# Optimization experiments

Measured on AMD Instinct MI355X. Metric: run time of the kernel, lower is better.

## Reference

```python
import jax, jax.numpy as jnp
import numpy as np
from jax import lax

L = 15      # time_conv_size
STRIDE = 2


def setup_inputs() -> dict:
    key = jax.random.key(0)
    k1, k2, k3 = jax.random.split(key, 3)
    x = jax.random.normal(k1, (8, 4096, 64), dtype=jnp.float32)
    w1 = jax.random.normal(k2, (L,), dtype=jnp.float32)
    w2 = jax.random.normal(k3, (L,), dtype=jnp.float32)
    return {"x": x, "w1": w1, "w2": w2}


def reference(x, w1, w2):
    # x: [B, T, C]; w1, w2: [L]
    B, T, C = x.shape
    p = L // 2
    # --- weighted local mean: mu[b,t,c] = sum_k w1[k] * x_pad[b,t+k,c] ---
    x_pad = jnp.pad(x, ((0, 0), (p, p), (0, 0)))
    mu = sum(w1[k] * x_pad[:, k:k + T, :] for k in range(L))  # [B,T,C]
    # --- centered diagonal bilinear (covariance) pooling ---
    xc_pad = jnp.pad(x - mu, ((0, 0), (p, p), (0, 0)))  # [B, T+2p, C]
    # strided window indices: I = ceil(T/STRIDE) windows of length L
    starts = jnp.arange(0, T, STRIDE)                   # [I]
    idx = starts[:, None] + jnp.arange(L)[None, :]      # [I, L]
    win = xc_pad[:, idx, :]                             # [B, I, L, C]
    sigma = jnp.einsum('bilc,l,bild->bicd', win, w2, win)
    I = starts.shape[0]
    sigma = sigma.reshape(B, I, C * C)
    mu_s = mu[:, ::STRIDE, :]                           # [B, I, C]
    out = jnp.concatenate([mu_s, sigma], axis=-1)       # [B, I, C + C*C]
    # K.l2_normalize over last axis (epsilon=1e-12)
    denom = lax.rsqrt(jnp.maximum(jnp.sum(out * out, axis=-1, keepdims=True), 1e-12))
    return out * denom
```

## Files before the change

kernel.cpp:

```cpp
#include <hip/hip_runtime.h>

#define Tdim 4096
#define Bdim 8
#define Cdim 64
#define Ldim 15
#define Idim 2048
#define OUTW 4160
#define G    2
#define RX   (2*G + 27)
#define RXC  (2*G + 13)
#define NBLK (Idim / G)

typedef float v4f __attribute__((ext_vector_type(4)));

__global__ __launch_bounds__(256, 6) void cbp_kernel(const float* __restrict__ x,
                                                     const float* __restrict__ w1,
                                                     const float* __restrict__ w2,
                                                     float* __restrict__ out) {
    __shared__ float xbuf[RX][64];
    __shared__ float xcs[RXC][64];
    __shared__ float mus[G][64];
    __shared__ float red[4][G];

    const int tid = threadIdx.x;
    const int blk = blockIdx.x;
    const int b  = blk >> 10;
    const int i0 = (blk & (NBLK - 1)) << 1;
    const int s0 = i0 << 1;

    const float* xb = x + (size_t)b * (Tdim * Cdim);
    for (int v = tid; v < RX * 16; v += 256) {
        const int r  = v >> 4;
        const int c4 = (v & 15) << 2;
        const int t  = s0 - 14 + r;
        float4 val = make_float4(0.f, 0.f, 0.f, 0.f);
        if (t >= 0 && t < Tdim) val = *(const float4*)(xb + (size_t)t * Cdim + c4);
        *(float4*)(&xbuf[r][c4]) = val;
    }
    __syncthreads();

    for (int v = tid; v < RXC * 16; v += 256) {
        const int j  = v >> 4;
        const int c4 = (v & 15) << 2;
        const int t  = s0 - 7 + j;
        float4 m = make_float4(0.f, 0.f, 0.f, 0.f);
#pragma unroll
        for (int k = 0; k < Ldim; ++k) {
            const float w = w1[k];
            const float4 xv = *(const float4*)(&xbuf[j + k][c4]);
            m.x = fmaf(w, xv.x, m.x);
            m.y = fmaf(w, xv.y, m.y);
            m.z = fmaf(w, xv.z, m.z);
            m.w = fmaf(w, xv.w, m.w);
        }
        const float4 xv = *(const float4*)(&xbuf[j + 7][c4]);
        float4 xc = make_float4(0.f, 0.f, 0.f, 0.f);
        if (t >= 0 && t < Tdim)
            xc = make_float4(xv.x - m.x, xv.y - m.y, xv.z - m.z, xv.w - m.w);
        *(float4*)(&xcs[j][c4]) = xc;
        if (j == 7 || j == 9)
            *(float4*)(&mus[(j - 7) >> 1][c4]) = m;
    }
    __syncthreads();

    const int c0 = (tid >> 4) << 2;
    const int d0 = (tid & 15) << 2;
    float acc[G][4][4];
#pragma unroll
    for (int g = 0; g < G; ++g)
#pragma unroll
        for (int cc = 0; cc < 4; ++cc)
#pragma unroll
            for (int dd = 0; dd < 4; ++dd) acc[g][cc][dd] = 0.f;

#pragma unroll
    for (int r = 0; r < RXC; ++r) {
        const float4 xd = *(const float4*)(&xcs[r][d0]);
        const float4 xc = *(const float4*)(&xcs[r][c0]);
#pragma unroll
        for (int g = 0; g < G; ++g) {
            const int l = r - 2 * g;
            if (l >= 0 && l < Ldim) {
                const float w  = w2[l];
                const float a0 = w * xc.x, a1 = w * xc.y, a2 = w * xc.z, a3 = w * xc.w;
                acc[g][0][0] = fmaf(a0, xd.x, acc[g][0][0]);
                acc[g][0][1] = fmaf(a0, xd.y, acc[g][0][1]);
                acc[g][0][2] = fmaf(a0, xd.z, acc[g][0][2]);
                acc[g][0][3] = fmaf(a0, xd.w, acc[g][0][3]);
                acc[g][1][0] = fmaf(a1, xd.x, acc[g][1][0]);
                acc[g][1][1] = fmaf(a1, xd.y, acc[g][1][1]);
                acc[g][1][2] = fmaf(a1, xd.z, acc[g][1][2]);
                acc[g][1][3] = fmaf(a1, xd.w, acc[g][1][3]);
                acc[g][2][0] = fmaf(a2, xd.x, acc[g][2][0]);
                acc[g][2][1] = fmaf(a2, xd.y, acc[g][2][1]);
                acc[g][2][2] = fmaf(a2, xd.z, acc[g][2][2]);
                acc[g][2][3] = fmaf(a2, xd.w, acc[g][2][3]);
                acc[g][3][0] = fmaf(a3, xd.x, acc[g][3][0]);
                acc[g][3][1] = fmaf(a3, xd.y, acc[g][3][1]);
                acc[g][3][2] = fmaf(a3, xd.z, acc[g][3][2]);
                acc[g][3][3] = fmaf(a3, xd.w, acc[g][3][3]);
            }
        }
    }

    float local[G];
#pragma unroll
    for (int g = 0; g < G; ++g) {
        float s = 0.f;
#pragma unroll
        for (int cc = 0; cc < 4; ++cc)
#pragma unroll
            for (int dd = 0; dd < 4; ++dd) s = fmaf(acc[g][cc][dd], acc[g][cc][dd], s);
        local[g] = s;
    }
    if (tid < Cdim) {
#pragma unroll
        for (int g = 0; g < G; ++g) local[g] = fmaf(mus[g][tid], mus[g][tid], local[g]);
    }
#pragma unroll
    for (int off = 32; off; off >>= 1)
#pragma unroll
        for (int g = 0; g < G; ++g) local[g] += __shfl_down(local[g], off, 64);
    if ((tid & 63) == 0) {
        const int w = tid >> 6;
#pragma unroll
        for (int g = 0; g < G; ++g) red[w][g] = local[g];
    }
    __syncthreads();

    float scale[G];
#pragma unroll
    for (int g = 0; g < G; ++g) {
        const float ss = red[0][g] + red[1][g] + red[2][g] + red[3][g];
        scale[g] = rsqrtf(fmaxf(ss, 1e-12f));
    }

#pragma unroll
    for (int g = 0; g < G; ++g) {
        const float sc = scale[g];
        float* orow = out + (size_t)(b * Idim + i0 + g) * OUTW;
        if (tid < 16) {
            const float4 m4 = *(const float4*)(&mus[g][tid << 2]);
            v4f mv = { m4.x * sc, m4.y * sc, m4.z * sc, m4.w * sc };
            __builtin_nontemporal_store(mv, (v4f*)(orow + (tid << 2)));
        }
        float* osig = orow + Cdim;
#pragma unroll
        for (int cc = 0; cc < 4; ++cc) {
            v4f v = { acc[g][cc][0] * sc, acc[g][cc][1] * sc,
                      acc[g][cc][2] * sc, acc[g][cc][3] * sc };
            __builtin_nontemporal_store(v, (v4f*)(osig + (c0 + cc) * Cdim + d0));
        }
    }
}

extern "C" void kernel_launch(void* const* d_in, const int* in_sizes, int n_in,
                              void* d_out, int out_size, void* d_ws, size_t ws_size,
                              hipStream_t stream) {
    const float* x  = (const float*)d_in[0];
    const float* w1 = (const float*)d_in[1];
    const float* w2 = (const float*)d_in[2];
    float* out = (float*)d_out;
    cbp_kernel<<<dim3(Bdim * NBLK), dim3(256), 0, stream>>>(x, w1, w2, out);
}
```

Before: 283.0 us.

## Make blocks persistent over eight window groups with register-prefetched input tiles

Each block now handles eight consecutive window-pair groups instead of one, so the grid shrinks from 8192 to 1024 blocks. The next group's input rows are loaded into registers at the start of the current group and written to shared memory after the centering pass. This overlaps global loads with compute and cuts block launch overhead. In exchange, parallelism drops, launch bounds go from 6 to 4 waves, and register pressure rises. The kernel is output-store bound, so the gain may be small.

```diff
diff --git a/kernel.cpp b/kernel.cpp
--- a/kernel.cpp
+++ b/kernel.cpp
@@ -7,13 +7,16 @@
 #define Idim 2048
 #define OUTW 4160
 #define G    2
-#define RX   (2*G + 27)
-#define RXC  (2*G + 13)
-#define NBLK (Idim / G)
+#define RX   31
+#define RXC  17
+#define NBLK 1024
+#define TOTALG 8192
+#define GRID  1024
+#define ITERS 8
 
 typedef float v4f __attribute__((ext_vector_type(4)));
 
-__global__ __launch_bounds__(256, 6) void cbp_kernel(const float* __restrict__ x,
+__global__ __launch_bounds__(256, 4) void cbp_kernel(const float* __restrict__ x,
                                                      const float* __restrict__ w1,
                                                      const float* __restrict__ w2,
                                                      float* __restrict__ out) {
@@ -24,132 +27,169 @@
 
     const int tid = threadIdx.x;
     const int blk = blockIdx.x;
-    const int b  = blk >> 10;
-    const int i0 = (blk & (NBLK - 1)) << 1;
-    const int s0 = i0 << 1;
-
-    const float* xb = x + (size_t)b * (Tdim * Cdim);
-    for (int v = tid; v < RX * 16; v += 256) {
-        const int r  = v >> 4;
-        const int c4 = (v & 15) << 2;
-        const int t  = s0 - 14 + r;
-        float4 val = make_float4(0.f, 0.f, 0.f, 0.f);
-        if (t >= 0 && t < Tdim) val = *(const float4*)(xb + (size_t)t * Cdim + c4);
-        *(float4*)(&xbuf[r][c4]) = val;
+
+    const int r0  = tid >> 4;
+    const int r1  = r0 + 16;
+    const int c4s = (tid & 15) << 2;
+
+    {
+        const int grp = blk * ITERS;
+        const int b   = grp >> 10;
+        const int s0  = (grp & (NBLK - 1)) << 2;
+        const float* xb = x + (size_t)b * (Tdim * Cdim);
+        const int t0 = s0 - 14 + r0;
+        const int t1 = s0 - 14 + r1;
+        float4 st0 = make_float4(0.f, 0.f, 0.f, 0.f);
+        float4 st1 = make_float4(0.f, 0.f, 0.f, 0.f);
+        if (t0 >= 0 && t0 < Tdim) st0 = *(const float4*)(xb + (size_t)t0 * Cdim + c4s);
+        if (tid < 240 && t1 >= 0 && t1 < Tdim)
+            st1 = *(const float4*)(xb + (size_t)t1 * Cdim + c4s);
+        *(float4*)(&xbuf[r0][c4s]) = st0;
+        if (tid < 240) *(float4*)(&xbuf[r1][c4s]) = st1;
     }
-    __syncthreads();
-
-    for (int v = tid; v < RXC * 16; v += 256) {
-        const int j  = v >> 4;
-        const int c4 = (v & 15) << 2;
-        const int t  = s0 - 7 + j;
-        float4 m = make_float4(0.f, 0.f, 0.f, 0.f);
-#pragma unroll
-        for (int k = 0; k < Ldim; ++k) {
-            const float w = w1[k];
-            const float4 xv = *(const float4*)(&xbuf[j + k][c4]);
-            m.x = fmaf(w, xv.x, m.x);
-            m.y = fmaf(w, xv.y, m.y);
-            m.z = fmaf(w, xv.z, m.z);
-            m.w = fmaf(w, xv.w, m.w);
-        }
-        const float4 xv = *(const float4*)(&xbuf[j + 7][c4]);
-        float4 xc = make_float4(0.f, 0.f, 0.f, 0.f);
-        if (t >= 0 && t < Tdim)
-            xc = make_float4(xv.x - m.x, xv.y - m.y, xv.z - m.z, xv.w - m.w);
-        *(float4*)(&xcs[j][c4]) = xc;
-        if (j == 7 || j == 9)
-            *(float4*)(&mus[(j - 7) >> 1][c4]) = m;
-    }
-    __syncthreads();
 
     const int c0 = (tid >> 4) << 2;
     const int d0 = (tid & 15) << 2;
-    float acc[G][4][4];
-#pragma unroll
-    for (int g = 0; g < G; ++g)
-#pragma unroll
-        for (int cc = 0; cc < 4; ++cc)
-#pragma unroll
-            for (int dd = 0; dd < 4; ++dd) acc[g][cc][dd] = 0.f;
-
-#pragma unroll
-    for (int r = 0; r < RXC; ++r) {
-        const float4 xd = *(const float4*)(&xcs[r][d0]);
-        const float4 xc = *(const float4*)(&xcs[r][c0]);
+
+#pragma unroll 1
+    for (int it = 0; it < ITERS; ++it) {
+        const int grp = blk * ITERS + it;
+        const int b   = grp >> 10;
+        const int i0  = (grp & (NBLK - 1)) << 1;
+        const int s0  = i0 << 1;
+
+        __syncthreads();
+
+        const bool pf = (it + 1 < ITERS);
+        float4 nst0 = make_float4(0.f, 0.f, 0.f, 0.f);
+        float4 nst1 = make_float4(0.f, 0.f, 0.f, 0.f);
+        if (pf) {
+            const int grpn = grp + 1;
+            const int bn   = grpn >> 10;
+            const int s0n  = (grpn & (NBLK - 1)) << 2;
+            const float* xbn = x + (size_t)bn * (Tdim * Cdim);
+            const int t0 = s0n - 14 + r0;
+            const int t1 = s0n - 14 + r1;
+            if (t0 >= 0 && t0 < Tdim) nst0 = *(const float4*)(xbn + (size_t)t0 * Cdim + c4s);
+            if (tid < 240 && t1 >= 0 && t1 < Tdim)
+                nst1 = *(const float4*)(xbn + (size_t)t1 * Cdim + c4s);
+        }
+
+        for (int v = tid; v < RXC * 16; v += 256) {
+            const int j  = v >> 4;
+            const int c4 = (v & 15) << 2;
+            const int t  = s0 - 7 + j;
+            float4 m = make_float4(0.f, 0.f, 0.f, 0.f);
+#pragma unroll
+            for (int k = 0; k < Ldim; ++k) {
+                const float w = w1[k];
+                const float4 xv = *(const float4*)(&xbuf[j + k][c4]);
+                m.x = fmaf(w, xv.x, m.x);
+                m.y = fmaf(w, xv.y, m.y);
+                m.z = fmaf(w, xv.z, m.z);
+                m.w = fmaf(w, xv.w, m.w);
+            }
+            const float4 xv = *(const float4*)(&xbuf[j + 7][c4]);
+            float4 xc = make_float4(0.f, 0.f, 0.f, 0.f);
+            if (t >= 0 && t < Tdim)
+                xc = make_float4(xv.x - m.x, xv.y - m.y, xv.z - m.z, xv.w - m.w);
+            *(float4*)(&xcs[j][c4]) = xc;
+            if (j == 7 || j == 9)
+                *(float4*)(&mus[(j - 7) >> 1][c4]) = m;
+        }
+        __syncthreads();
+
+        if (pf) {
+            *(float4*)(&xbuf[r0][c4s]) = nst0;
+            if (tid < 240) *(float4*)(&xbuf[r1][c4s]) = nst1;
+        }
+
+        float acc[G][4][4];
+#pragma unroll
+        for (int g = 0; g < G; ++g)
+#pragma unroll
+            for (int cc = 0; cc < 4; ++cc)
+#pragma unroll
+                for (int dd = 0; dd < 4; ++dd) acc[g][cc][dd] = 0.f;
+
+#pragma unroll
+        for (int r = 0; r < RXC; ++r) {
+            const float4 xd = *(const float4*)(&xcs[r][d0]);
+            const float4 xc = *(const float4*)(&xcs[r][c0]);
+#pragma unroll
+            for (int g = 0; g < G; ++g) {
+                const int l = r - 2 * g;
+                if (l >= 0 && l < Ldim) {
+                    const float w  = w2[l];
+                    const float a0 = w * xc.x, a1 = w * xc.y, a2 = w * xc.z, a3 = w * xc.w;
+                    acc[g][0][0] = fmaf(a0, xd.x, acc[g][0][0]);
+                    acc[g][0][1] = fmaf(a0, xd.y, acc[g][0][1]);
+                    acc[g][0][2] = fmaf(a0, xd.z, acc[g][0][2]);
+                    acc[g][0][3] = fmaf(a0, xd.w, acc[g][0][3]);
+                    acc[g][1][0] = fmaf(a1, xd.x, acc[g][1][0]);
+                    acc[g][1][1] = fmaf(a1, xd.y, acc[g][1][1]);
+                    acc[g][1][2] = fmaf(a1, xd.z, acc[g][1][2]);
+                    acc[g][1][3] = fmaf(a1, xd.w, acc[g][1][3]);
+                    acc[g][2][0] = fmaf(a2, xd.x, acc[g][2][0]);
+                    acc[g][2][1] = fmaf(a2, xd.y, acc[g][2][1]);
+                    acc[g][2][2] = fmaf(a2, xd.z, acc[g][2][2]);
+                    acc[g][2][3] = fmaf(a2, xd.w, acc[g][2][3]);
+                    acc[g][3][0] = fmaf(a3, xd.x, acc[g][3][0]);
+                    acc[g][3][1] = fmaf(a3, xd.y, acc[g][3][1]);
+                    acc[g][3][2] = fmaf(a3, xd.z, acc[g][3][2]);
+                    acc[g][3][3] = fmaf(a3, xd.w, acc[g][3][3]);
+                }
+            }
+        }
+
+        float local[G];
 #pragma unroll
         for (int g = 0; g < G; ++g) {
-            const int l = r - 2 * g;
-            if (l >= 0 && l < Ldim) {
-                const float w  = w2[l];
-                const float a0 = w * xc.x, a1 = w * xc.y, a2 = w * xc.z, a3 = w * xc.w;
-                acc[g][0][0] = fmaf(a0, xd.x, acc[g][0][0]);
-                acc[g][0][1] = fmaf(a0, xd.y, acc[g][0][1]);
-                acc[g][0][2] = fmaf(a0, xd.z, acc[g][0][2]);
-                acc[g][0][3] = fmaf(a0, xd.w, acc[g][0][3]);
-                acc[g][1][0] = fmaf(a1, xd.x, acc[g][1][0]);
-                acc[g][1][1] = fmaf(a1, xd.y, acc[g][1][1]);
-                acc[g][1][2] = fmaf(a1, xd.z, acc[g][1][2]);
-                acc[g][1][3] = fmaf(a1, xd.w, acc[g][1][3]);
-                acc[g][2][0] = fmaf(a2, xd.x, acc[g][2][0]);
-                acc[g][2][1] = fmaf(a2, xd.y, acc[g][2][1]);
-                acc[g][2][2] = fmaf(a2, xd.z, acc[g][2][2]);
-                acc[g][2][3] = fmaf(a2, xd.w, acc[g][2][3]);
-                acc[g][3][0] = fmaf(a3, xd.x, acc[g][3][0]);
-                acc[g][3][1] = fmaf(a3, xd.y, acc[g][3][1]);
-                acc[g][3][2] = fmaf(a3, xd.z, acc[g][3][2]);
-                acc[g][3][3] = fmaf(a3, xd.w, acc[g][3][3]);
-            }
-        }
-    }
-
-    float local[G];
-#pragma unroll
-    for (int g = 0; g < G; ++g) {
-        float s = 0.f;
-#pragma unroll
-        for (int cc = 0; cc < 4; ++cc)
-#pragma unroll
-            for (int dd = 0; dd < 4; ++dd) s = fmaf(acc[g][cc][dd], acc[g][cc][dd], s);
-        local[g] = s;
-    }
-    if (tid < Cdim) {
-#pragma unroll
-        for (int g = 0; g < G; ++g) local[g] = fmaf(mus[g][tid], mus[g][tid], local[g]);
-    }
-#pragma unroll
-    for (int off = 32; off; off >>= 1)
-#pragma unroll
-        for (int g = 0; g < G; ++g) local[g] += __shfl_down(local[g], off, 64);
-    if ((tid & 63) == 0) {
-        const int w = tid >> 6;
-#pragma unroll
-        for (int g = 0; g < G; ++g) red[w][g] = local[g];
-    }
-    __syncthreads();
-
-    float scale[G];
-#pragma unroll
-    for (int g = 0; g < G; ++g) {
-        const float ss = red[0][g] + red[1][g] + red[2][g] + red[3][g];
-        scale[g] = rsqrtf(fmaxf(ss, 1e-12f));
-    }
-
-#pragma unroll
-    for (int g = 0; g < G; ++g) {
-        const float sc = scale[g];
-        float* orow = out + (size_t)(b * Idim + i0 + g) * OUTW;
-        if (tid < 16) {
-            const float4 m4 = *(const float4*)(&mus[g][tid << 2]);
-            v4f mv = { m4.x * sc, m4.y * sc, m4.z * sc, m4.w * sc };
-            __builtin_nontemporal_store(mv, (v4f*)(orow + (tid << 2)));
-        }
-        float* osig = orow + Cdim;
-#pragma unroll
-        for (int cc = 0; cc < 4; ++cc) {
-            v4f v = { acc[g][cc][0] * sc, acc[g][cc][1] * sc,
-                      acc[g][cc][2] * sc, acc[g][cc][3] * sc };
-            __builtin_nontemporal_store(v, (v4f*)(osig + (c0 + cc) * Cdim + d0));
+            float s = 0.f;
+#pragma unroll
+            for (int cc = 0; cc < 4; ++cc)
+#pragma unroll
+                for (int dd = 0; dd < 4; ++dd) s = fmaf(acc[g][cc][dd], acc[g][cc][dd], s);
+            local[g] = s;
+        }
+        if (tid < Cdim) {
+#pragma unroll
+            for (int g = 0; g < G; ++g) local[g] = fmaf(mus[g][tid], mus[g][tid], local[g]);
+        }
+#pragma unroll
+        for (int off = 32; off; off >>= 1)
+#pragma unroll
+            for (int g = 0; g < G; ++g) local[g] += __shfl_down(local[g], off, 64);
+        if ((tid & 63) == 0) {
+            const int w = tid >> 6;
+#pragma unroll
+            for (int g = 0; g < G; ++g) red[w][g] = local[g];
+        }
+        __syncthreads();
+
+        float scale[G];
+#pragma unroll
+        for (int g = 0; g < G; ++g) {
+            const float ss = red[0][g] + red[1][g] + red[2][g] + red[3][g];
+            scale[g] = rsqrtf(fmaxf(ss, 1e-12f));
+        }
+
+#pragma unroll
+        for (int g = 0; g < G; ++g) {
+            const float sc = scale[g];
+            float* orow = out + (size_t)(b * Idim + i0 + g) * OUTW;
+            if (tid < 16) {
+                const float4 m4 = *(const float4*)(&mus[g][tid << 2]);
+                v4f mv = { m4.x * sc, m4.y * sc, m4.z * sc, m4.w * sc };
+                __builtin_nontemporal_store(mv, (v4f*)(orow + (tid << 2)));
+            }
+            float* osig = orow + Cdim;
+#pragma unroll
+            for (int cc = 0; cc < 4; ++cc) {
+                v4f v = { acc[g][cc][0] * sc, acc[g][cc][1] * sc,
+                          acc[g][cc][2] * sc, acc[g][cc][3] * sc };
+                __builtin_nontemporal_store(v, (v4f*)(osig + (c0 + cc) * Cdim + d0));
+            }
         }
     }
 }
@@ -161,5 +201,5 @@
     const float* w1 = (const float*)d_in[1];
     const float* w2 = (const float*)d_in[2];
     float* out = (float*)d_out;
-    cbp_kernel<<<dim3(Bdim * NBLK), dim3(256), 0, stream>>>(x, w1, w2, out);
+    cbp_kernel<<<dim3(GRID), dim3(256), 0, stream>>>(x, w1, w2, out);
 }
```

Measured after the change: 289.6 us. 1.02x slower.
